# Kernel tuning notes

Hardware: AMD Instinct MI355X
Metric: run time of the kernel (lower is better)

The kernel has to match this reference:

```python
import jax, jax.numpy as jnp
import numpy as np

IN_FEATURES = 4096
OUT_FEATURES = 11008


def setup_inputs() -> dict:
    key = jax.random.key(0)
    kx, kw, ks, kb = jax.random.split(key, 4)
    x = jax.random.normal(kx, (64, IN_FEATURES), dtype=jnp.float32)
    # int8 quantized weight, stored as int32 for portability (values in [-128, 127])
    weight_quantized = jax.random.randint(kw, (OUT_FEATURES, IN_FEATURES), -128, 128, dtype=jnp.int32)
    # per-tensor scale, as produced by quantize_weights_int8: |w|.max()/127
    weight_scale = jnp.asarray(0.01, dtype=jnp.float32)
    bias = jax.random.normal(kb, (OUT_FEATURES,), dtype=jnp.float32) * 0.02
    return {"x": x, "weight_quantized": weight_quantized, "weight_scale": weight_scale, "bias": bias}


def reference(x, weight_quantized, weight_scale, bias):
    # dequantize_weights_int8: q.float() * scale, then F.linear(x, W, b) = x @ W.T + b
    weight = weight_quantized.astype(jnp.float32) * weight_scale  # [out, in]
    return jnp.einsum('mi,oi->mo', x, weight) + bias
```

## Files before the change

kernel.cpp:

```cpp
#include <hip/hip_runtime.h>


#define M_DIM 64
#define N_DIM 11008
#define K_DIM 4096
#define BLOCK_N 16
#define NBLOCKS (N_DIM / BLOCK_N)
#define KW (K_DIM / 4)

typedef __attribute__((ext_vector_type(8))) short bf16x8;
typedef __attribute__((ext_vector_type(8))) short s16x8;
typedef __attribute__((ext_vector_type(4))) float f32x4;
typedef __attribute__((ext_vector_type(4))) int i32x4;
typedef __attribute__((ext_vector_type(4))) short s16x4;

__device__ __forceinline__ short i2bf(int q) {
    float f = (float)q;
    return (short)(__builtin_bit_cast(unsigned int, f) >> 16);
}

__device__ __forceinline__ short f2bf(float f) {
    unsigned int u = __builtin_bit_cast(unsigned int, f);
    u = u + 0x7FFFu + ((u >> 16) & 1u);
    return (short)(u >> 16);
}

__global__ __launch_bounds__(256) void xcvt_kernel(const float* __restrict__ x,
                                                   short* __restrict__ xbf) {
    int idx = (blockIdx.x * 256 + threadIdx.x) * 8;
    f32x4 a = *(const f32x4*)(x + idx);
    f32x4 b = *(const f32x4*)(x + idx + 4);
    s16x8 h;
    h[0] = f2bf(a.x); h[1] = f2bf(a.y); h[2] = f2bf(a.z); h[3] = f2bf(a.w);
    h[4] = f2bf(b.x); h[5] = f2bf(b.y); h[6] = f2bf(b.z); h[7] = f2bf(b.w);
    *(s16x8*)(xbf + idx) = h;
}

__global__ __launch_bounds__(256) void qlinear_fused_kernel(const short* __restrict__ xbf,
                                                            const int* __restrict__ wq,
                                                            const float* __restrict__ scale_p,
                                                            const float* __restrict__ bias,
                                                            float* __restrict__ out) {
    __shared__ float red[4][M_DIM][BLOCK_N];

    const int tid  = threadIdx.x;
    const int wave = tid >> 6;
    const int lane = tid & 63;
    const int quad = lane >> 4;
    const int l16  = lane & 15;

    const int n0 = blockIdx.x * BLOCK_N;
    const int k0 = wave * KW;

    const int*   bptr = wq  + (size_t)(n0 + l16) * K_DIM + k0 + quad * 8;
    const short* aptr = xbf + (size_t)l16 * K_DIM + k0 + quad * 8;

    f32x4 acc[4] = {f32x4{0,0,0,0}, f32x4{0,0,0,0}, f32x4{0,0,0,0}, f32x4{0,0,0,0}};

    #pragma unroll 4
    for (int kk = 0; kk < KW; kk += 32) {
        i32x4 b0 = *(const i32x4*)(bptr + kk);
        i32x4 b1 = *(const i32x4*)(bptr + kk + 4);
        bf16x8 bfrag;
        bfrag[0] = i2bf(b0.x); bfrag[1] = i2bf(b0.y);
        bfrag[2] = i2bf(b0.z); bfrag[3] = i2bf(b0.w);
        bfrag[4] = i2bf(b1.x); bfrag[5] = i2bf(b1.y);
        bfrag[6] = i2bf(b1.z); bfrag[7] = i2bf(b1.w);

        #pragma unroll
        for (int mi = 0; mi < 4; ++mi) {
            bf16x8 afrag = *(const bf16x8*)(aptr + (size_t)mi * 16 * K_DIM + kk);
            acc[mi] = __builtin_amdgcn_mfma_f32_16x16x32_bf16(afrag, bfrag, acc[mi], 0, 0, 0);
        }
    }

    #pragma unroll
    for (int mi = 0; mi < 4; ++mi) {
        #pragma unroll
        for (int r = 0; r < 4; ++r) {
            red[wave][mi * 16 + quad * 4 + r][l16] = acc[mi][r];
        }
    }
    __syncthreads();

    {
        const float scale = *scale_p;
        int idx = tid * 4;
        int m = idx >> 4;
        int n = idx & 15;
        f32x4 s0 = *(const f32x4*)&red[0][m][n];
        f32x4 s1 = *(const f32x4*)&red[1][m][n];
        f32x4 s2 = *(const f32x4*)&red[2][m][n];
        f32x4 s3 = *(const f32x4*)&red[3][m][n];
        f32x4 bb = *(const f32x4*)(bias + n0 + n);
        f32x4 r;
        r.x = (s0.x + s1.x + s2.x + s3.x) * scale + bb.x;
        r.y = (s0.y + s1.y + s2.y + s3.y) * scale + bb.y;
        r.z = (s0.z + s1.z + s2.z + s3.z) * scale + bb.z;
        r.w = (s0.w + s1.w + s2.w + s3.w) * scale + bb.w;
        *(f32x4*)(out + (size_t)m * N_DIM + n0 + n) = r;
    }
}


#define KSPLIT 8
#define KC (K_DIM / KSPLIT)
#define BK 128
#define LDS_STRIDE 136
#define FB_BLOCK_N 64

__global__ __launch_bounds__(256) void init_bias_kernel(const float* __restrict__ bias,
                                                        float* __restrict__ out) {
    int idx = blockIdx.x * 256 + threadIdx.x;
    int col4 = idx % 2752;
    f32x4 b = *(const f32x4*)(bias + col4 * 4);
    *(f32x4*)(out + (size_t)idx * 4) = b;
}

__global__ __launch_bounds__(256) void qlinear_atomic_kernel(const float* __restrict__ x,
                                                             const int* __restrict__ wq,
                                                             const float* __restrict__ scale_p,
                                                             float* __restrict__ out) {
    __shared__ short lds[M_DIM * LDS_STRIDE];

    const int tid  = threadIdx.x;
    const int wave = tid >> 6;
    const int lane = tid & 63;
    const int quad = lane >> 4;
    const int l16  = lane & 15;

    const int n0  = blockIdx.x * FB_BLOCK_N;
    const int kc0 = blockIdx.y * KC;
    const float scale = *scale_p;

    const int nw = n0 + wave * 16 + l16;
    const int* wptr = wq + (size_t)nw * K_DIM + kc0 + quad * 8;

    f32x4 acc[4] = {f32x4{0,0,0,0}, f32x4{0,0,0,0}, f32x4{0,0,0,0}, f32x4{0,0,0,0}};

    for (int kb = 0; kb < KC; kb += BK) {
        {
            const float* xbase = x + kc0 + kb;
            #pragma unroll
            for (int j = 0; j < 8; ++j) {
                int f  = tid + j * 256;
                int row = f >> 5;
                int c4  = f & 31;
                f32x4 v = *(const f32x4*)(xbase + (size_t)row * K_DIM + c4 * 4);
                s16x4 h;
                h.x = f2bf(v.x); h.y = f2bf(v.y); h.z = f2bf(v.z); h.w = f2bf(v.w);
                *(s16x4*)&lds[row * LDS_STRIDE + c4 * 4] = h;
            }
        }
        __syncthreads();

        #pragma unroll
        for (int kk = 0; kk < BK; kk += 32) {
            i32x4 b0 = *(const i32x4*)(wptr + kb + kk);
            i32x4 b1 = *(const i32x4*)(wptr + kb + kk + 4);
            bf16x8 bfrag;
            bfrag[0] = i2bf(b0.x); bfrag[1] = i2bf(b0.y);
            bfrag[2] = i2bf(b0.z); bfrag[3] = i2bf(b0.w);
            bfrag[4] = i2bf(b1.x); bfrag[5] = i2bf(b1.y);
            bfrag[6] = i2bf(b1.z); bfrag[7] = i2bf(b1.w);

            #pragma unroll
            for (int mi = 0; mi < 4; ++mi) {
                bf16x8 afrag = *(const bf16x8*)&lds[(mi * 16 + l16) * LDS_STRIDE + kk + quad * 8];
                acc[mi] = __builtin_amdgcn_mfma_f32_16x16x32_bf16(afrag, bfrag, acc[mi], 0, 0, 0);
            }
        }
        __syncthreads();
    }

    const int nout = n0 + wave * 16 + l16;
    #pragma unroll
    for (int mi = 0; mi < 4; ++mi) {
        #pragma unroll
        for (int r = 0; r < 4; ++r) {
            int m = mi * 16 + quad * 4 + r;
            atomicAdd(&out[(size_t)m * N_DIM + nout], acc[mi][r] * scale);
        }
    }
}

extern "C" void kernel_launch(void* const* d_in, const int* in_sizes, int n_in,
                              void* d_out, int out_size, void* d_ws, size_t ws_size,
                              hipStream_t stream) {
    const float* x      = (const float*)d_in[0];
    const int*   wq     = (const int*)d_in[1];
    const float* scale  = (const float*)d_in[2];
    const float* bias   = (const float*)d_in[3];
    float* out = (float*)d_out;

    const size_t xbf_bytes = (size_t)M_DIM * K_DIM * sizeof(short);

    if (ws_size >= xbf_bytes && d_ws != nullptr) {
        short* xbf = (short*)d_ws;
        xcvt_kernel<<<(M_DIM * K_DIM) / (256 * 8), 256, 0, stream>>>(x, xbf);
        qlinear_fused_kernel<<<NBLOCKS, 256, 0, stream>>>(xbf, wq, scale, bias, out);
    } else {
        init_bias_kernel<<<688, 256, 0, stream>>>(bias, out);
        dim3 grid(N_DIM / FB_BLOCK_N, KSPLIT);
        qlinear_atomic_kernel<<<grid, 256, 0, stream>>>(x, wq, scale, out);
    }
}
```

Baseline: 285.2 us.

## Double-buffer weight tiles via direct global-to-LDS loads with swizzle

Replaces the direct per-lane global weight loads in the main GEMV-like kernel with per-wave double-buffered LDS staging using global_load_lds, with an XOR swizzle to avoid bank conflicts. Activation fragments are prefetched into registers one tile ahead, and explicit vmcnt waits plus scheduling barriers overlap the next tile's loads with the current tile's MFMA work. The goal is to hide the memory latency of streaming the int32 weights, the dominant traffic. The hand-counted vmcnt thresholds are fragile and depend on the exact load count per stage.

New measurement: 268.1 us. -6.0%, faster.

```diff
diff --git a/kernel.cpp b/kernel.cpp
--- a/kernel.cpp
+++ b/kernel.cpp
@@ -7,6 +7,9 @@
 #define BLOCK_N 16
 #define NBLOCKS (N_DIM / BLOCK_N)
 #define KW (K_DIM / 4)
+#define BK 64
+#define NT (KW / BK)
+#define WTILE_B (16 * 256)
 
 typedef __attribute__((ext_vector_type(8))) short bf16x8;
 typedef __attribute__((ext_vector_type(8))) short s16x8;
@@ -23,6 +26,13 @@
     unsigned int u = __builtin_bit_cast(unsigned int, f);
     u = u + 0x7FFFu + ((u >> 16) & 1u);
     return (short)(u >> 16);
+}
+
+__device__ __forceinline__ void load_lds_16B(const void* g, void* l) {
+    __builtin_amdgcn_global_load_lds(
+        (const __attribute__((address_space(1))) unsigned int*)g,
+        (__attribute__((address_space(3))) unsigned int*)l,
+        16, 0, 0);
 }
 
 __global__ __launch_bounds__(256) void xcvt_kernel(const float* __restrict__ x,
@@ -36,12 +46,53 @@
     *(s16x8*)(xbf + idx) = h;
 }
 
-__global__ __launch_bounds__(256) void qlinear_fused_kernel(const short* __restrict__ xbf,
-                                                            const int* __restrict__ wq,
-                                                            const float* __restrict__ scale_p,
-                                                            const float* __restrict__ bias,
-                                                            float* __restrict__ out) {
-    __shared__ float red[4][M_DIM][BLOCK_N];
+__device__ __forceinline__ void stage_w(const int* __restrict__ wq, int n0, int kA,
+                                        char* wl, int lane) {
+    #pragma unroll
+    for (int j = 0; j < 4; ++j) {
+        int row  = j * 4 + (lane >> 4);
+        int colb = ((lane & 15) * 16) ^ ((row & 7) << 4);
+        const char* g = (const char*)(wq + (size_t)(n0 + row) * K_DIM + kA) + colb;
+        load_lds_16B(g, wl + j * 1024);
+    }
+}
+
+__device__ __forceinline__ void xpref(const short* __restrict__ xbf, int kA,
+                                      int l16, int quad, bf16x8 (&xb)[8]) {
+    #pragma unroll
+    for (int i = 0; i < 8; ++i) {
+        int mi = i & 3;
+        int kk = (i >> 2) * 32;
+        xb[i] = *(const bf16x8*)(xbf + (size_t)(mi * 16 + l16) * K_DIM + kA + kk + quad * 8);
+    }
+}
+
+__device__ __forceinline__ void compute_t(const char* wl, const bf16x8 (&xb)[8],
+                                          f32x4 (&acc)[4], int l16, int quad) {
+    const int wsw = (l16 & 7) << 4;
+    #pragma unroll
+    for (int h = 0; h < 2; ++h) {
+        const int L0 = (h * 32 + quad * 8) * 4;
+        i32x4 b0 = *(const i32x4*)(wl + l16 * 256 + ((L0)      ^ wsw));
+        i32x4 b1 = *(const i32x4*)(wl + l16 * 256 + ((L0 + 16) ^ wsw));
+        bf16x8 bfrag;
+        bfrag[0] = i2bf(b0.x); bfrag[1] = i2bf(b0.y);
+        bfrag[2] = i2bf(b0.z); bfrag[3] = i2bf(b0.w);
+        bfrag[4] = i2bf(b1.x); bfrag[5] = i2bf(b1.y);
+        bfrag[6] = i2bf(b1.z); bfrag[7] = i2bf(b1.w);
+        #pragma unroll
+        for (int mi = 0; mi < 4; ++mi) {
+            acc[mi] = __builtin_amdgcn_mfma_f32_16x16x32_bf16(xb[h * 4 + mi], bfrag, acc[mi], 0, 0, 0);
+        }
+    }
+}
+
+__global__ __launch_bounds__(256) void qlinear_v6_kernel(const short* __restrict__ xbf,
+                                                         const int* __restrict__ wq,
+                                                         const float* __restrict__ scale_p,
+                                                         const float* __restrict__ bias,
+                                                         float* __restrict__ out) {
+    __shared__ char smem[4 * 2 * WTILE_B];
 
     const int tid  = threadIdx.x;
     const int wave = tid >> 6;
@@ -52,46 +103,57 @@
     const int n0 = blockIdx.x * BLOCK_N;
     const int k0 = wave * KW;
 
-    const int*   bptr = wq  + (size_t)(n0 + l16) * K_DIM + k0 + quad * 8;
-    const short* aptr = xbf + (size_t)l16 * K_DIM + k0 + quad * 8;
+    char* buf0 = smem + wave * 2 * WTILE_B;
+    char* buf1 = buf0 + WTILE_B;
 
     f32x4 acc[4] = {f32x4{0,0,0,0}, f32x4{0,0,0,0}, f32x4{0,0,0,0}, f32x4{0,0,0,0}};
-
-    #pragma unroll 4
-    for (int kk = 0; kk < KW; kk += 32) {
-        i32x4 b0 = *(const i32x4*)(bptr + kk);
-        i32x4 b1 = *(const i32x4*)(bptr + kk + 4);
-        bf16x8 bfrag;
-        bfrag[0] = i2bf(b0.x); bfrag[1] = i2bf(b0.y);
-        bfrag[2] = i2bf(b0.z); bfrag[3] = i2bf(b0.w);
-        bfrag[4] = i2bf(b1.x); bfrag[5] = i2bf(b1.y);
-        bfrag[6] = i2bf(b1.z); bfrag[7] = i2bf(b1.w);
-
-        #pragma unroll
-        for (int mi = 0; mi < 4; ++mi) {
-            bf16x8 afrag = *(const bf16x8*)(aptr + (size_t)mi * 16 * K_DIM + kk);
-            acc[mi] = __builtin_amdgcn_mfma_f32_16x16x32_bf16(afrag, bfrag, acc[mi], 0, 0, 0);
-        }
-    }
-
+    bf16x8 xa[8], xb[8];
+
+    xpref(xbf, k0, l16, quad, xa);
+    stage_w(wq, n0, k0, buf0, lane);
+
+    for (int t = 0; t < NT - 2; t += 2) {
+        xpref(xbf, k0 + (t + 1) * BK, l16, quad, xb);
+        stage_w(wq, n0, k0 + (t + 1) * BK, buf1, lane);
+        asm volatile("s_waitcnt vmcnt(12)" ::: "memory");
+        __builtin_amdgcn_sched_barrier(0);
+        compute_t(buf0, xa, acc, l16, quad);
+
+        xpref(xbf, k0 + (t + 2) * BK, l16, quad, xa);
+        stage_w(wq, n0, k0 + (t + 2) * BK, buf0, lane);
+        asm volatile("s_waitcnt vmcnt(12)" ::: "memory");
+        __builtin_amdgcn_sched_barrier(0);
+        compute_t(buf1, xb, acc, l16, quad);
+    }
+    xpref(xbf, k0 + (NT - 1) * BK, l16, quad, xb);
+    stage_w(wq, n0, k0 + (NT - 1) * BK, buf1, lane);
+    asm volatile("s_waitcnt vmcnt(12)" ::: "memory");
+    __builtin_amdgcn_sched_barrier(0);
+    compute_t(buf0, xa, acc, l16, quad);
+    asm volatile("s_waitcnt vmcnt(0)" ::: "memory");
+    __builtin_amdgcn_sched_barrier(0);
+    compute_t(buf1, xb, acc, l16, quad);
+
+    __syncthreads();
+    float* red = (float*)smem;
     #pragma unroll
     for (int mi = 0; mi < 4; ++mi) {
         #pragma unroll
         for (int r = 0; r < 4; ++r) {
-            red[wave][mi * 16 + quad * 4 + r][l16] = acc[mi][r];
+            int m = mi * 16 + quad * 4 + r;
+            red[(wave * M_DIM + m) * BLOCK_N + l16] = acc[mi][r];
         }
     }
     __syncthreads();
-
     {
         const float scale = *scale_p;
         int idx = tid * 4;
         int m = idx >> 4;
         int n = idx & 15;
-        f32x4 s0 = *(const f32x4*)&red[0][m][n];
-        f32x4 s1 = *(const f32x4*)&red[1][m][n];
-        f32x4 s2 = *(const f32x4*)&red[2][m][n];
-        f32x4 s3 = *(const f32x4*)&red[3][m][n];
+        f32x4 s0 = *(const f32x4*)&red[(0 * M_DIM + m) * BLOCK_N + n];
+        f32x4 s1 = *(const f32x4*)&red[(1 * M_DIM + m) * BLOCK_N + n];
+        f32x4 s2 = *(const f32x4*)&red[(2 * M_DIM + m) * BLOCK_N + n];
+        f32x4 s3 = *(const f32x4*)&red[(3 * M_DIM + m) * BLOCK_N + n];
         f32x4 bb = *(const f32x4*)(bias + n0 + n);
         f32x4 r;
         r.x = (s0.x + s1.x + s2.x + s3.x) * scale + bb.x;
@@ -102,10 +164,9 @@
     }
 }
 
-
 #define KSPLIT 8
 #define KC (K_DIM / KSPLIT)
-#define BK 128
+#define FB_BK 128
 #define LDS_STRIDE 136
 #define FB_BLOCK_N 64
 
@@ -138,7 +199,7 @@
 
     f32x4 acc[4] = {f32x4{0,0,0,0}, f32x4{0,0,0,0}, f32x4{0,0,0,0}, f32x4{0,0,0,0}};
 
-    for (int kb = 0; kb < KC; kb += BK) {
+    for (int kb = 0; kb < KC; kb += FB_BK) {
         {
             const float* xbase = x + kc0 + kb;
             #pragma unroll
@@ -155,7 +216,7 @@
         __syncthreads();
 
         #pragma unroll
-        for (int kk = 0; kk < BK; kk += 32) {
+        for (int kk = 0; kk < FB_BK; kk += 32) {
             i32x4 b0 = *(const i32x4*)(wptr + kb + kk);
             i32x4 b1 = *(const i32x4*)(wptr + kb + kk + 4);
             bf16x8 bfrag;
@@ -198,7 +259,7 @@
     if (ws_size >= xbf_bytes && d_ws != nullptr) {
         short* xbf = (short*)d_ws;
         xcvt_kernel<<<(M_DIM * K_DIM) / (256 * 8), 256, 0, stream>>>(x, xbf);
-        qlinear_fused_kernel<<<NBLOCKS, 256, 0, stream>>>(xbf, wq, scale, bias, out);
+        qlinear_v6_kernel<<<NBLOCKS, 256, 0, stream>>>(xbf, wq, scale, bias, out);
     } else {
         init_bias_kernel<<<688, 256, 0, stream>>>(bias, out);
         dim3 grid(N_DIM / FB_BLOCK_N, KSPLIT);
```
